# Kernel optimization log

Hardware: AMD Instinct MI355X
Metric: run time of the kernel (lower is better)

Reference implementation:

```python
import jax, jax.numpy as jnp
import numpy as np

N_HEADS = 32
D_IN = 128 + 256 + 1024  # 1408
D_HID = 256
D_OUT = 3


def setup_inputs() -> dict:
    key = jax.random.key(0)
    k1, k2, k3, k4, k5 = jax.random.split(key, 5)
    B = 16384
    total_feat = jax.random.normal(k1, (B, D_IN), dtype=jnp.float32)
    # Stacked per-head parameters. Original zero-inits the second Linear;
    # we use small random values so the baseline exercises non-trivial math.
    s1 = 1.0 / np.sqrt(D_IN)
    s2 = 1.0 / np.sqrt(D_HID)
    W1 = jax.random.uniform(k2, (N_HEADS, D_IN, D_HID), jnp.float32, -s1, s1)
    b1 = jax.random.uniform(k3, (N_HEADS, D_HID), jnp.float32, -s1, s1)
    W2 = jax.random.uniform(k4, (N_HEADS, D_HID, D_OUT), jnp.float32, -s2, s2)
    b2 = jax.random.uniform(k5, (N_HEADS, D_OUT), jnp.float32, -s2, s2)
    return {"total_feat": total_feat, "W1": W1, "b1": b1, "W2": W2, "b2": b2}


def reference(total_feat, W1, b1, W2, b2):
    # 32 heads of Linear(1408->256) -> ReLU -> Linear(256->3), batched.
    h = jax.nn.relu(jnp.einsum('bf,hfo->bho', total_feat, W1) + b1)  # [B,32,256]
    out = jnp.einsum('bho,hop->bhp', h, W2) + b2                     # [B,32,3]
    B = total_feat.shape[0]
    # concat(dim=-1) over heads == reshape since each head emits 3 contiguous values
    return out.reshape(B, N_HEADS * D_OUT)                           # [B,96]
```

## Files before the change

### kernel.cpp

```cpp
#include <hip/hip_runtime.h>
#include <hip/hip_bf16.h>
#include <stdint.h>

#define D_IN    1408
#define D_HID   256
#define N_HEADS 32
#define BATCH   16384

#define BM 128
#define BN 256
#define BK 32
#define KTILES (D_IN / BK)
#define NSEG 8

typedef unsigned short u16;
typedef short short8 __attribute__((ext_vector_type(8)));
typedef float f32x4 __attribute__((ext_vector_type(4)));

__device__ __forceinline__ u16 f2b(float f) {
  __hip_bfloat16 h = __float2bfloat16(f);
  return *(u16*)&h;
}

__device__ __forceinline__ void gload_lds16(const void* g, void* l) {
  __builtin_amdgcn_global_load_lds(
      (const __attribute__((address_space(1))) uint32_t*)((const uint32_t*)g),
      (__attribute__((address_space(3))) uint32_t*)((uint32_t*)l),
      16, 0, 0);
}

#define CONV_BLOCKS 22528
__global__ void prep(const float4* __restrict__ X, ushort4* __restrict__ Xb,
                     const float* __restrict__ W1, u16* __restrict__ W1T) {
  const int bid = blockIdx.x;
  const int tid = threadIdx.x;
  if (bid < CONV_BLOCKS) {
    int i = bid * 256 + tid;
    float4 v = X[i];
    ushort4 o;
    o.x = f2b(v.x); o.y = f2b(v.y); o.z = f2b(v.z); o.w = f2b(v.w);
    Xb[i] = o;
    return;
  }
  __shared__ u16 tile[64][68];
  const int b  = bid - CONV_BLOCKS;
  const int f0 = (b % 22) * 64;
  const int o0 = ((b / 22) & 3) * 64;
  const int h  = b / 88;
  const int tx = tid & 63;
  const int ty = tid >> 6;
  const size_t ib = (size_t)h * D_IN * D_HID;
  #pragma unroll
  for (int i = ty; i < 64; i += 4)
    tile[i][tx] = f2b(W1[ib + (size_t)(f0 + i) * D_HID + o0 + tx]);
  __syncthreads();
  const size_t ob = (size_t)h * D_HID * D_IN;
  #pragma unroll
  for (int pass = 0; pass < 4; ++pass) {
    int r = pass * 16 + ty * 4 + (tx >> 4);
    int c = (tx & 15) * 4;
    ushort4 v;
    v.x = tile[c + 0][r]; v.y = tile[c + 1][r];
    v.z = tile[c + 2][r]; v.w = tile[c + 3][r];
    *(ushort4*)&W1T[ob + (size_t)(o0 + r) * D_IN + f0 + c] = v;
  }
}

__global__ __launch_bounds__(512, 4) void mano_gemm(
    const u16* __restrict__ X,
    const u16* __restrict__ W1T,
    const float* __restrict__ b1,
    const float* __restrict__ W2,
    const float* __restrict__ b2,
    float* __restrict__ out)
{
  __shared__ __align__(16) u16 As[2][BM * BK];
  __shared__ __align__(16) u16 Bs[2][BN * BK];
  __shared__ __align__(16) float scr[1536];
  __shared__ float b1L[256];
  __shared__ float w2L[768];
  __shared__ float b2L[3];

  const int tid  = threadIdx.x;
  const int lane = tid & 63;
  const int wid  = tid >> 6;
  const int quad = lane >> 4;
  const int l15  = lane & 15;
  const int wm   = wid >> 2;
  const int wn   = wid & 3;

  const int bid  = blockIdx.x;
  const int head = (bid & 7) * 4 + ((bid >> 3) & 3);
  const int u    = bid >> 5;

  const u16* Bu = W1T + (size_t)head * D_HID * D_IN;

  if (tid < 256) b1L[tid] = b1[head * D_HID + tid];
  for (int i = tid; i < 768; i += 512) w2L[i] = W2[(size_t)head * D_HID * 3 + i];
  if (tid < 3)  b2L[tid] = b2[head * 3 + tid];

  int aoff;
  {
    int row = tid >> 2, c = tid & 3;
    aoff = row * D_IN + (c ^ ((row >> 1) & 3)) * 8;
  }
  int boff[2];
  #pragma unroll
  for (int cc = 0; cc < 2; ++cc) {
    int ci = cc * 512 + tid;
    int row = ci >> 2, c = ci & 3;
    boff[cc] = row * D_IN + (c ^ ((row >> 1) & 3)) * 8;
  }

  const int p16 = (quad ^ ((l15 >> 1) & 3)) * 16;
  const int abase = (wm * 64 + l15) * 64 + p16;
  const int bbase = (wn * 64 + l15) * 64 + p16;

#define STG(BI, AP, BP) do {                                                   \
    gload_lds16((AP) + aoff, &As[BI][wid * 512]);                              \
    _Pragma("unroll")                                                          \
    for (int cc = 0; cc < 2; ++cc)                                             \
      gload_lds16((BP) + boff[cc], &Bs[BI][(cc * 512 + wid * 64) * 8]);        \
  } while (0)

  f32x4 acc[4][4];
  #pragma unroll
  for (int i = 0; i < 4; ++i)
    #pragma unroll
    for (int j = 0; j < 4; ++j)
      acc[i][j] = f32x4{0.f, 0.f, 0.f, 0.f};

  short8 a[4], b[4];

#define TILE(BI, AP, BP, SK) do {                                              \
    if (!(SK)) STG((BI) ^ 1, AP, BP);                                          \
    _Pragma("unroll") for (int mf = 0; mf < 4; ++mf)                           \
      a[mf] = *(const short8*)((const char*)&As[BI][0] + abase + mf * 1024);   \
    _Pragma("unroll") for (int nf = 0; nf < 4; ++nf)                           \
      b[nf] = *(const short8*)((const char*)&Bs[BI][0] + bbase + nf * 1024);   \
    __builtin_amdgcn_s_setprio(1);                                             \
    _Pragma("unroll") for (int mf = 0; mf < 4; ++mf)                           \
      _Pragma("unroll") for (int nf = 0; nf < 4; ++nf)                         \
        acc[mf][nf] = __builtin_amdgcn_mfma_f32_16x16x32_bf16(                 \
            a[mf], b[nf], acc[mf][nf], 0, 0, 0);                               \
    __builtin_amdgcn_s_setprio(0);                                             \
    asm volatile("s_waitcnt vmcnt(0)" ::: "memory");                           \
    __builtin_amdgcn_s_barrier();                                              \
  } while (0)

  {
    const u16* A0 = X + (size_t)(u * BM) * D_IN;
    STG(0, A0, Bu);
    asm volatile("s_waitcnt lgkmcnt(0)" ::: "memory");
    asm volatile("s_waitcnt vmcnt(0)" ::: "memory");
    __builtin_amdgcn_s_barrier();
  }

  #pragma unroll 1
  for (int g = 0; g < NSEG; ++g) {
    const u16* AuC = X + (size_t)((g * 16 + u) * BM) * D_IN;
    const u16* AuN = AuC + (size_t)(16 * BM) * D_IN;
    const bool lastseg = (g == NSEG - 1);

    #pragma unroll 1
    for (int j = 0; j < KTILES / 2; ++j) {
      const int kt1 = 2 * j + 1;
      const int kt2 = 2 * j + 2;
      const bool wrap = (kt2 >= KTILES);
      const int k2m  = wrap ? 0 : kt2;
      const u16* Ap1 = AuC + kt1 * BK;
      const u16* Bp1 = Bu + kt1 * BK;
      const u16* Ap2 = (wrap ? AuN : AuC) + k2m * BK;
      const u16* Bp2 = Bu + k2m * BK;
      const bool sk2 = lastseg && wrap;

      TILE(0, Ap1, Bp1, false);
      TILE(1, Ap2, Bp2, sk2);
    }

    {
      float b1v[4], w2v[4][3];
      #pragma unroll
      for (int nf = 0; nf < 4; ++nf) {
        int col = wn * 64 + nf * 16 + l15;
        b1v[nf] = b1L[col];
        #pragma unroll
        for (int p = 0; p < 3; ++p) w2v[nf][p] = w2L[col * 3 + p];
      }
      const int m0 = (g * 16 + u) * BM;

      #pragma unroll
      for (int mf = 0; mf < 4; ++mf) {
        float ps[4][3];
        #pragma unroll
        for (int r = 0; r < 4; ++r)
          #pragma unroll
          for (int p = 0; p < 3; ++p) ps[r][p] = 0.f;

        #pragma unroll
        for (int nf = 0; nf < 4; ++nf)
          #pragma unroll
          for (int r = 0; r < 4; ++r) {
            float h = acc[mf][nf][r] + b1v[nf];
            h = h > 0.f ? h : 0.f;
            #pragma unroll
            for (int p = 0; p < 3; ++p)
              ps[r][p] = fmaf(h, w2v[nf][p], ps[r][p]);
          }

        #pragma unroll
        for (int mask = 1; mask < 16; mask <<= 1)
          #pragma unroll
          for (int r = 0; r < 4; ++r)
            #pragma unroll
            for (int p = 0; p < 3; ++p)
              ps[r][p] += __shfl_xor(ps[r][p], mask, 64);

        if (l15 == 0) {
          int row = wm * 64 + mf * 16 + quad * 4;
          #pragma unroll
          for (int r = 0; r < 4; ++r)
            #pragma unroll
            for (int p = 0; p < 3; ++p)
              scr[((row + r) * 3 + p) * 4 + wn] = ps[r][p];
        }
      }
      asm volatile("s_waitcnt lgkmcnt(0)" ::: "memory");
      __builtin_amdgcn_s_barrier();

      for (int i = tid; i < BM * 3; i += 512) {
        int row = i / 3, p = i - row * 3;
        float v = scr[i * 4 + 0] + scr[i * 4 + 1] + scr[i * 4 + 2]
                + scr[i * 4 + 3] + b2L[p];
        out[(size_t)(m0 + row) * (N_HEADS * 3) + head * 3 + p] = v;
      }

      #pragma unroll
      for (int i = 0; i < 4; ++i)
        #pragma unroll
        for (int jj = 0; jj < 4; ++jj)
          acc[i][jj] = f32x4{0.f, 0.f, 0.f, 0.f};
    }
  }

#undef STG
#undef TILE
}

extern "C" void kernel_launch(void* const* d_in, const int* in_sizes, int n_in,
                              void* d_out, int out_size, void* d_ws, size_t ws_size,
                              hipStream_t stream) {
  const float* X  = (const float*)d_in[0];
  const float* W1 = (const float*)d_in[1];
  const float* b1 = (const float*)d_in[2];
  const float* W2 = (const float*)d_in[3];
  const float* b2 = (const float*)d_in[4];

  u16* Xb  = (u16*)d_ws;
  u16* W1T = (u16*)((char*)d_ws + (size_t)BATCH * D_IN * 2);

  prep<<<CONV_BLOCKS + (D_IN / 64) * (D_HID / 64) * N_HEADS, 256, 0, stream>>>(
      (const float4*)X, (ushort4*)Xb, W1, W1T);

  mano_gemm<<<dim3(512), 512, 0, stream>>>(
      Xb, W1T, b1, W2, b2, (float*)d_out);
}
```

Measured before the change: 574.3 us.

## Enlarge GEMM block tile to 256x256x64 with 4 waves of 128x128 each

```diff
diff --git a/kernel.cpp b/kernel.cpp
--- a/kernel.cpp
+++ b/kernel.cpp
@@ -7,9 +7,9 @@
 #define N_HEADS 32
 #define BATCH   16384
 
-#define BM 128
+#define BM 256
 #define BN 256
-#define BK 32
+#define BK 64
 #define KTILES (D_IN / BK)
 #define NSEG 8
 
@@ -66,7 +66,7 @@
   }
 }
 
-__global__ __launch_bounds__(512, 4) void mano_gemm(
+__global__ __launch_bounds__(256, 1) void mano_gemm(
     const u16* __restrict__ X,
     const u16* __restrict__ W1T,
     const float* __restrict__ b1,
@@ -86,71 +86,83 @@
   const int wid  = tid >> 6;
   const int quad = lane >> 4;
   const int l15  = lane & 15;
-  const int wm   = wid >> 2;
-  const int wn   = wid & 3;
+  const int wm   = wid >> 1;
+  const int wn   = wid & 1;
 
   const int bid  = blockIdx.x;
   const int head = (bid & 7) * 4 + ((bid >> 3) & 3);
-  const int u    = bid >> 5;
+  const int u2   = bid >> 5;
 
   const u16* Bu = W1T + (size_t)head * D_HID * D_IN;
 
-  if (tid < 256) b1L[tid] = b1[head * D_HID + tid];
-  for (int i = tid; i < 768; i += 512) w2L[i] = W2[(size_t)head * D_HID * 3 + i];
-  if (tid < 3)  b2L[tid] = b2[head * 3 + tid];
-
-  int aoff;
-  {
-    int row = tid >> 2, c = tid & 3;
-    aoff = row * D_IN + (c ^ ((row >> 1) & 3)) * 8;
-  }
-  int boff[2];
-  #pragma unroll
-  for (int cc = 0; cc < 2; ++cc) {
-    int ci = cc * 512 + tid;
-    int row = ci >> 2, c = ci & 3;
-    boff[cc] = row * D_IN + (c ^ ((row >> 1) & 3)) * 8;
-  }
-
-  const int p16 = (quad ^ ((l15 >> 1) & 3)) * 16;
-  const int abase = (wm * 64 + l15) * 64 + p16;
-  const int bbase = (wn * 64 + l15) * 64 + p16;
-
-#define STG(BI, AP, BP) do {                                                   \
-    gload_lds16((AP) + aoff, &As[BI][wid * 512]);                              \
-    _Pragma("unroll")                                                          \
-    for (int cc = 0; cc < 2; ++cc)                                             \
-      gload_lds16((BP) + boff[cc], &Bs[BI][(cc * 512 + wid * 64) * 8]);        \
-  } while (0)
-
-  f32x4 acc[4][4];
-  #pragma unroll
-  for (int i = 0; i < 4; ++i)
+  b1L[tid] = b1[head * D_HID + tid];
+  #pragma unroll
+  for (int i = tid; i < 768; i += 256) w2L[i] = W2[(size_t)head * D_HID * 3 + i];
+  if (tid < 3) b2L[tid] = b2[head * 3 + tid];
+
+  int soff[8];
+  #pragma unroll
+  for (int c = 0; c < 8; ++c) {
+    int ci  = c * 256 + tid;
+    int row = ci >> 3;
+    int k8  = (ci & 7) ^ (row & 7);
+    soff[c] = row * D_IN + k8 * 8;
+  }
+
+#define STG_A(BI, P) do { _Pragma("unroll")                                    \
+    for (int c = 0; c < 8; ++c)                                                \
+      gload_lds16((P) + soff[c], &As[BI][(c * 256 + wid * 64) * 8]); } while (0)
+#define STG_B(BI, P) do { _Pragma("unroll")                                    \
+    for (int c = 0; c < 8; ++c)                                                \
+      gload_lds16((P) + soff[c], &Bs[BI][(c * 256 + wid * 64) * 8]); } while (0)
+
+  const int rx  = l15 & 7;
+  const int co0 = (quad ^ rx) * 16;
+  const int co1 = ((4 + quad) ^ rx) * 16;
+  const int aro = (wm * 128 + l15) * 128;
+  const int bro = (wn * 128 + l15) * 128;
+
+#define LDA(BI, mf, CO) \
+  (*(const short8*)((const char*)&As[BI][0] + aro + (mf) * 2048 + (CO)))
+#define LDB(BI, nf, CO) \
+  (*(const short8*)((const char*)&Bs[BI][0] + bro + (nf) * 2048 + (CO)))
+
+  f32x4 acc[8][8];
+  #pragma unroll
+  for (int i = 0; i < 8; ++i)
     #pragma unroll
-    for (int j = 0; j < 4; ++j)
+    for (int j = 0; j < 8; ++j)
       acc[i][j] = f32x4{0.f, 0.f, 0.f, 0.f};
 
-  short8 a[4], b[4];
-
-#define TILE(BI, AP, BP, SK) do {                                              \
-    if (!(SK)) STG((BI) ^ 1, AP, BP);                                          \
-    _Pragma("unroll") for (int mf = 0; mf < 4; ++mf)                           \
-      a[mf] = *(const short8*)((const char*)&As[BI][0] + abase + mf * 1024);   \
-    _Pragma("unroll") for (int nf = 0; nf < 4; ++nf)                           \
-      b[nf] = *(const short8*)((const char*)&Bs[BI][0] + bbase + nf * 1024);   \
+  short8 fa0[8], fb0[8], fa1[8], fb1[8];
+
+#define TILE(BI, APn, BPn, SK) do {                                            \
+    _Pragma("unroll") for (int m = 0; m < 8; ++m) fa0[m] = LDA(BI, m, co0);    \
+    _Pragma("unroll") for (int n = 0; n < 8; ++n) fb0[n] = LDB(BI, n, co0);    \
+    _Pragma("unroll") for (int m = 0; m < 8; ++m) fa1[m] = LDA(BI, m, co1);    \
+    _Pragma("unroll") for (int n = 0; n < 8; ++n) fb1[n] = LDB(BI, n, co1);    \
+    if (!(SK)) STG_A((BI) ^ 1, APn);                                           \
     __builtin_amdgcn_s_setprio(1);                                             \
-    _Pragma("unroll") for (int mf = 0; mf < 4; ++mf)                           \
-      _Pragma("unroll") for (int nf = 0; nf < 4; ++nf)                         \
-        acc[mf][nf] = __builtin_amdgcn_mfma_f32_16x16x32_bf16(                 \
-            a[mf], b[nf], acc[mf][nf], 0, 0, 0);                               \
+    _Pragma("unroll") for (int m = 0; m < 8; ++m)                              \
+      _Pragma("unroll") for (int n = 0; n < 8; ++n)                            \
+        acc[m][n] = __builtin_amdgcn_mfma_f32_16x16x32_bf16(                   \
+            fa0[m], fb0[n], acc[m][n], 0, 0, 0);                               \
+    __builtin_amdgcn_s_setprio(0);                                             \
+    if (!(SK)) STG_B((BI) ^ 1, BPn);                                           \
+    __builtin_amdgcn_s_setprio(1);                                             \
+    _Pragma("unroll") for (int m = 0; m < 8; ++m)                              \
+      _Pragma("unroll") for (int n = 0; n < 8; ++n)                            \
+        acc[m][n] = __builtin_amdgcn_mfma_f32_16x16x32_bf16(                   \
+            fa1[m], fb1[n], acc[m][n], 0, 0, 0);                               \
     __builtin_amdgcn_s_setprio(0);                                             \
     asm volatile("s_waitcnt vmcnt(0)" ::: "memory");                           \
     __builtin_amdgcn_s_barrier();                                              \
   } while (0)
 
   {
-    const u16* A0 = X + (size_t)(u * BM) * D_IN;
-    STG(0, A0, Bu);
+    const u16* A0 = X + (size_t)(u2 * BM) * D_IN;
+    STG_A(0, A0);
+    STG_B(0, Bu);
     asm volatile("s_waitcnt lgkmcnt(0)" ::: "memory");
     asm volatile("s_waitcnt vmcnt(0)" ::: "memory");
     __builtin_amdgcn_s_barrier();
@@ -158,39 +170,32 @@
 
   #pragma unroll 1
   for (int g = 0; g < NSEG; ++g) {
-    const u16* AuC = X + (size_t)((g * 16 + u) * BM) * D_IN;
-    const u16* AuN = AuC + (size_t)(16 * BM) * D_IN;
+    const u16* AuC = X + (size_t)((g * 8 + u2) * BM) * D_IN;
+    const u16* AuN = AuC + (size_t)(8 * BM) * D_IN;
     const bool lastseg = (g == NSEG - 1);
 
     #pragma unroll 1
     for (int j = 0; j < KTILES / 2; ++j) {
-      const int kt1 = 2 * j + 1;
-      const int kt2 = 2 * j + 2;
-      const bool wrap = (kt2 >= KTILES);
-      const int k2m  = wrap ? 0 : kt2;
-      const u16* Ap1 = AuC + kt1 * BK;
-      const u16* Bp1 = Bu + kt1 * BK;
-      const u16* Ap2 = (wrap ? AuN : AuC) + k2m * BK;
-      const u16* Bp2 = Bu + k2m * BK;
-      const bool sk2 = lastseg && wrap;
-
-      TILE(0, Ap1, Bp1, false);
-      TILE(1, Ap2, Bp2, sk2);
+      TILE(0, AuC + (2 * j + 1) * BK, Bu + (2 * j + 1) * BK, false);
+      const bool wrap = (j == KTILES / 2 - 1);
+      const u16* Ap2 = wrap ? AuN : AuC + (2 * j + 2) * BK;
+      const u16* Bp2 = Bu + (wrap ? 0 : (2 * j + 2)) * BK;
+      TILE(1, Ap2, Bp2, lastseg && wrap);
     }
 
     {
-      float b1v[4], w2v[4][3];
-      #pragma unroll
-      for (int nf = 0; nf < 4; ++nf) {
-        int col = wn * 64 + nf * 16 + l15;
-        b1v[nf] = b1L[col];
-        #pragma unroll
-        for (int p = 0; p < 3; ++p) w2v[nf][p] = w2L[col * 3 + p];
+      float b1v[8], w2v[8][3];
+      #pragma unroll
+      for (int n = 0; n < 8; ++n) {
+        int col = wn * 128 + n * 16 + l15;
+        b1v[n] = b1L[col];
+        #pragma unroll
+        for (int p = 0; p < 3; ++p) w2v[n][p] = w2L[col * 3 + p];
       }
-      const int m0 = (g * 16 + u) * BM;
-
-      #pragma unroll
-      for (int mf = 0; mf < 4; ++mf) {
+      const int m0 = (g * 8 + u2) * BM;
+
+      #pragma unroll
+      for (int m = 0; m < 8; ++m) {
         float ps[4][3];
         #pragma unroll
         for (int r = 0; r < 4; ++r)
@@ -198,14 +203,14 @@
           for (int p = 0; p < 3; ++p) ps[r][p] = 0.f;
 
         #pragma unroll
-        for (int nf = 0; nf < 4; ++nf)
+        for (int n = 0; n < 8; ++n)
           #pragma unroll
           for (int r = 0; r < 4; ++r) {
-            float h = acc[mf][nf][r] + b1v[nf];
+            float h = acc[m][n][r] + b1v[n];
             h = h > 0.f ? h : 0.f;
             #pragma unroll
             for (int p = 0; p < 3; ++p)
-              ps[r][p] = fmaf(h, w2v[nf][p], ps[r][p]);
+              ps[r][p] = fmaf(h, w2v[n][p], ps[r][p]);
           }
 
         #pragma unroll
@@ -217,33 +222,36 @@
               ps[r][p] += __shfl_xor(ps[r][p], mask, 64);
 
         if (l15 == 0) {
-          int row = wm * 64 + mf * 16 + quad * 4;
+          int row = wm * 128 + m * 16 + quad * 4;
           #pragma unroll
           for (int r = 0; r < 4; ++r)
             #pragma unroll
             for (int p = 0; p < 3; ++p)
-              scr[((row + r) * 3 + p) * 4 + wn] = ps[r][p];
+              scr[((row + r) * 3 + p) * 2 + wn] = ps[r][p];
         }
       }
       asm volatile("s_waitcnt lgkmcnt(0)" ::: "memory");
       __builtin_amdgcn_s_barrier();
 
-      for (int i = tid; i < BM * 3; i += 512) {
+      #pragma unroll
+      for (int i = tid; i < BM * 3; i += 256) {
         int row = i / 3, p = i - row * 3;
-        float v = scr[i * 4 + 0] + scr[i * 4 + 1] + scr[i * 4 + 2]
-                + scr[i * 4 + 3] + b2L[p];
-        out[(size_t)(m0 + row) * (N_HEADS * 3) + head * 3 + p] = v;
+        out[(size_t)(m0 + row) * (N_HEADS * 3) + head * 3 + p] =
+            scr[i * 2] + scr[i * 2 + 1] + b2L[p];
       }
 
       #pragma unroll
-      for (int i = 0; i < 4; ++i)
-        #pragma unroll
-        for (int jj = 0; jj < 4; ++jj)
+      for (int i = 0; i < 8; ++i)
+        #pragma unroll
+        for (int jj = 0; jj < 8; ++jj)
           acc[i][jj] = f32x4{0.f, 0.f, 0.f, 0.f};
     }
   }
 
-#undef STG
+#undef STG_A
+#undef STG_B
+#undef LDA
+#undef LDB
 #undef TILE
 }
 
@@ -262,6 +270,6 @@
   prep<<<CONV_BLOCKS + (D_IN / 64) * (D_HID / 64) * N_HEADS, 256, 0, stream>>>(
       (const float4*)X, (ushort4*)Xb, W1, W1T);
 
-  mano_gemm<<<dim3(512), 512, 0, stream>>>(
+  mano_gemm<<<dim3(256), 256, 0, stream>>>(
       Xb, W1T, b1, W2, b2, (float*)d_out);
 }
```

After: 1.022 ms. 1.78x slower.

## Triple-buffer LDS tiles with prefetch distance two and partial vmcnt waits

Applied to the files above, without the earlier changes.

```diff
diff --git a/kernel.cpp b/kernel.cpp
--- a/kernel.cpp
+++ b/kernel.cpp
@@ -12,6 +12,7 @@
 #define BK 32
 #define KTILES (D_IN / BK)
 #define NSEG 8
+#define BUFU16 (BM * BK + BN * BK)
 
 typedef unsigned short u16;
 typedef short short8 __attribute__((ext_vector_type(8)));
@@ -74,9 +75,7 @@
     const float* __restrict__ b2,
     float* __restrict__ out)
 {
-  __shared__ __align__(16) u16 As[2][BM * BK];
-  __shared__ __align__(16) u16 Bs[2][BN * BK];
-  __shared__ __align__(16) float scr[1536];
+  __shared__ __align__(16) u16 tiles[3][BUFU16];
   __shared__ float b1L[256];
   __shared__ float w2L[768];
   __shared__ float b2L[3];
@@ -94,6 +93,7 @@
   const int u    = bid >> 5;
 
   const u16* Bu = W1T + (size_t)head * D_HID * D_IN;
+  u16* lds = &tiles[0][0];
 
   if (tid < 256) b1L[tid] = b1[head * D_HID + tid];
   for (int i = tid; i < 768; i += 512) w2L[i] = W2[(size_t)head * D_HID * 3 + i];
@@ -116,11 +116,12 @@
   const int abase = (wm * 64 + l15) * 64 + p16;
   const int bbase = (wn * 64 + l15) * 64 + p16;
 
-#define STG(BI, AP, BP) do {                                                   \
-    gload_lds16((AP) + aoff, &As[BI][wid * 512]);                              \
+#define STG(BUFP, AP, BP) do {                                                 \
+    gload_lds16((AP) + aoff, (BUFP) + wid * 512);                              \
     _Pragma("unroll")                                                          \
     for (int cc = 0; cc < 2; ++cc)                                             \
-      gload_lds16((BP) + boff[cc], &Bs[BI][(cc * 512 + wid * 64) * 8]);        \
+      gload_lds16((BP) + boff[cc],                                             \
+                  (BUFP) + 4096 + cc * 4096 + wid * 512);                      \
   } while (0)
 
   f32x4 acc[4][4];
@@ -132,29 +133,16 @@
 
   short8 a[4], b[4];
 
-#define TILE(BI, AP, BP, SK) do {                                              \
-    if (!(SK)) STG((BI) ^ 1, AP, BP);                                          \
-    _Pragma("unroll") for (int mf = 0; mf < 4; ++mf)                           \
-      a[mf] = *(const short8*)((const char*)&As[BI][0] + abase + mf * 1024);   \
-    _Pragma("unroll") for (int nf = 0; nf < 4; ++nf)                           \
-      b[nf] = *(const short8*)((const char*)&Bs[BI][0] + bbase + nf * 1024);   \
-    __builtin_amdgcn_s_setprio(1);                                             \
-    _Pragma("unroll") for (int mf = 0; mf < 4; ++mf)                           \
-      _Pragma("unroll") for (int nf = 0; nf < 4; ++nf)                         \
-        acc[mf][nf] = __builtin_amdgcn_mfma_f32_16x16x32_bf16(                 \
-            a[mf], b[nf], acc[mf][nf], 0, 0, 0);                               \
-    __builtin_amdgcn_s_setprio(0);                                             \
-    asm volatile("s_waitcnt vmcnt(0)" ::: "memory");                           \
-    __builtin_amdgcn_s_barrier();                                              \
-  } while (0)
-
   {
     const u16* A0 = X + (size_t)(u * BM) * D_IN;
-    STG(0, A0, Bu);
+    STG(lds, A0, Bu);
+    STG(lds + BUFU16, A0 + BK, Bu + BK);
     asm volatile("s_waitcnt lgkmcnt(0)" ::: "memory");
-    asm volatile("s_waitcnt vmcnt(0)" ::: "memory");
+    asm volatile("s_waitcnt vmcnt(3)" ::: "memory");
     __builtin_amdgcn_s_barrier();
   }
+
+  int bq = 0;
 
   #pragma unroll 1
   for (int g = 0; g < NSEG; ++g) {
@@ -163,22 +151,46 @@
     const bool lastseg = (g == NSEG - 1);
 
     #pragma unroll 1
-    for (int j = 0; j < KTILES / 2; ++j) {
-      const int kt1 = 2 * j + 1;
-      const int kt2 = 2 * j + 2;
-      const bool wrap = (kt2 >= KTILES);
-      const int k2m  = wrap ? 0 : kt2;
-      const u16* Ap1 = AuC + kt1 * BK;
-      const u16* Bp1 = Bu + kt1 * BK;
-      const u16* Ap2 = (wrap ? AuN : AuC) + k2m * BK;
-      const u16* Bp2 = Bu + k2m * BK;
-      const bool sk2 = lastseg && wrap;
-
-      TILE(0, Ap1, Bp1, false);
-      TILE(1, Ap2, Bp2, sk2);
+    for (int kt = 0; kt < KTILES; ++kt) {
+      int k2 = kt + 2;
+      const u16* Ab2 = AuC;
+      bool skip = false;
+      if (k2 >= KTILES) { k2 -= KTILES; Ab2 = AuN; skip = lastseg; }
+      const bool drain = lastseg && (kt >= KTILES - 2);
+
+      int bq2 = bq + 2; if (bq2 >= 3) bq2 -= 3;
+      u16* bufC = lds + bq * BUFU16;
+      u16* bufN = lds + bq2 * BUFU16;
+
+      if (!skip) STG(bufN, Ab2 + k2 * BK, Bu + k2 * BK);
+
+      #pragma unroll
+      for (int mf = 0; mf < 4; ++mf)
+        a[mf] = *(const short8*)((const char*)bufC + abase + mf * 1024);
+      #pragma unroll
+      for (int nf = 0; nf < 4; ++nf)
+        b[nf] = *(const short8*)((const char*)bufC + 8192 + bbase + nf * 1024);
+
+      __builtin_amdgcn_s_setprio(1);
+      #pragma unroll
+      for (int mf = 0; mf < 4; ++mf)
+        #pragma unroll
+        for (int nf = 0; nf < 4; ++nf)
+          acc[mf][nf] = __builtin_amdgcn_mfma_f32_16x16x32_bf16(
+              a[mf], b[nf], acc[mf][nf], 0, 0, 0);
+      __builtin_amdgcn_s_setprio(0);
+
+      if (drain) { asm volatile("s_waitcnt vmcnt(0)" ::: "memory"); }
+      else       { asm volatile("s_waitcnt vmcnt(3)" ::: "memory"); }
+      __builtin_amdgcn_s_barrier();
+
+      bq = bq + 1; if (bq >= 3) bq -= 3;
     }
 
     {
+      int bqf = bq + 2; if (bqf >= 3) bqf -= 3;
+      float* scr = (float*)(lds + bqf * BUFU16);
+
       float b1v[4], w2v[4][3];
       #pragma unroll
       for (int nf = 0; nf < 4; ++nf) {
@@ -234,6 +246,7 @@
                 + scr[i * 4 + 3] + b2L[p];
         out[(size_t)(m0 + row) * (N_HEADS * 3) + head * 3 + p] = v;
       }
+      asm volatile("s_waitcnt lgkmcnt(0)" ::: "memory");
 
       #pragma unroll
       for (int i = 0; i < 4; ++i)
@@ -244,7 +257,6 @@
   }
 
 #undef STG
-#undef TILE
 }
 
 extern "C" void kernel_launch(void* const* d_in, const int* in_sizes, int n_in,
```

Measured after the change: 590.0 us. +2.7%, slower.

## Double GEMM M tile and K step, load weights directly into registers

Applied to the files above, without the earlier changes.

```diff
diff --git a/kernel.cpp b/kernel.cpp
--- a/kernel.cpp
+++ b/kernel.cpp
@@ -7,9 +7,9 @@
 #define N_HEADS 32
 #define BATCH   16384
 
-#define BM 128
+#define BM 256
 #define BN 256
-#define BK 32
+#define BK 64
 #define KTILES (D_IN / BK)
 #define NSEG 8
 
@@ -66,7 +66,7 @@
   }
 }
 
-__global__ __launch_bounds__(512, 4) void mano_gemm(
+__global__ __launch_bounds__(512, 2) void mano_gemm(
     const u16* __restrict__ X,
     const u16* __restrict__ W1T,
     const float* __restrict__ b1,
@@ -75,8 +75,7 @@
     float* __restrict__ out)
 {
   __shared__ __align__(16) u16 As[2][BM * BK];
-  __shared__ __align__(16) u16 Bs[2][BN * BK];
-  __shared__ __align__(16) float scr[1536];
+  __shared__ __align__(16) float scr[3072];
   __shared__ float b1L[256];
   __shared__ float w2L[768];
   __shared__ float b2L[3];
@@ -91,7 +90,7 @@
 
   const int bid  = blockIdx.x;
   const int head = (bid & 7) * 4 + ((bid >> 3) & 3);
-  const int u    = bid >> 5;
+  const int u2   = bid >> 5;
 
   const u16* Bu = W1T + (size_t)head * D_HID * D_IN;
 
@@ -99,58 +98,72 @@
   for (int i = tid; i < 768; i += 512) w2L[i] = W2[(size_t)head * D_HID * 3 + i];
   if (tid < 3)  b2L[tid] = b2[head * 3 + tid];
 
-  int aoff;
-  {
-    int row = tid >> 2, c = tid & 3;
-    aoff = row * D_IN + (c ^ ((row >> 1) & 3)) * 8;
-  }
-  int boff[2];
-  #pragma unroll
-  for (int cc = 0; cc < 2; ++cc) {
-    int ci = cc * 512 + tid;
-    int row = ci >> 2, c = ci & 3;
-    boff[cc] = row * D_IN + (c ^ ((row >> 1) & 3)) * 8;
-  }
-
-  const int p16 = (quad ^ ((l15 >> 1) & 3)) * 16;
-  const int abase = (wm * 64 + l15) * 64 + p16;
-  const int bbase = (wn * 64 + l15) * 64 + p16;
-
-#define STG(BI, AP, BP) do {                                                   \
-    gload_lds16((AP) + aoff, &As[BI][wid * 512]);                              \
-    _Pragma("unroll")                                                          \
-    for (int cc = 0; cc < 2; ++cc)                                             \
-      gload_lds16((BP) + boff[cc], &Bs[BI][(cc * 512 + wid * 64) * 8]);        \
-  } while (0)
-
-  f32x4 acc[4][4];
-  #pragma unroll
-  for (int i = 0; i < 4; ++i)
+  int soff[4];
+  #pragma unroll
+  for (int c = 0; c < 4; ++c) {
+    int ci  = c * 512 + tid;
+    int row = ci >> 3;
+    int k8  = (ci & 7) ^ (row & 7);
+    soff[c] = row * D_IN + k8 * 8;
+  }
+
+#define STG_A(BI, P) do { _Pragma("unroll")                                    \
+    for (int c = 0; c < 4; ++c)                                                \
+      gload_lds16((P) + soff[c], &As[BI][(c * 512 + wid * 64) * 8]); } while (0)
+
+  const int wm16l = wm * 16 + l15;
+  const int rx  = l15 & 7;
+  const int co0 = (quad ^ rx) * 16;
+  const int co1 = ((4 + quad) ^ rx) * 16;
+
+#define LDAF(BI, mf, CO)                                                       \
+  (*(const short8*)((const char*)&As[BI][0] + ((mf) * 32 + wm16l) * 128 + (CO)))
+
+  int bgo[4];
+  #pragma unroll
+  for (int nf = 0; nf < 4; ++nf)
+    bgo[nf] = (nf * 64 + wn * 16 + l15) * D_IN + quad * 8;
+
+  f32x4 acc[8][4];
+  #pragma unroll
+  for (int i = 0; i < 8; ++i)
     #pragma unroll
     for (int j = 0; j < 4; ++j)
       acc[i][j] = f32x4{0.f, 0.f, 0.f, 0.f};
 
-  short8 a[4], b[4];
-
-#define TILE(BI, AP, BP, SK) do {                                              \
-    if (!(SK)) STG((BI) ^ 1, AP, BP);                                          \
-    _Pragma("unroll") for (int mf = 0; mf < 4; ++mf)                           \
-      a[mf] = *(const short8*)((const char*)&As[BI][0] + abase + mf * 1024);   \
+  short8 a[8];
+  short8 bA[4][2], bB[4][2];
+
+#define TILE(BI, APn, SKA, BCUR, BNXT, KTB) do {                               \
     _Pragma("unroll") for (int nf = 0; nf < 4; ++nf)                           \
-      b[nf] = *(const short8*)((const char*)&Bs[BI][0] + bbase + nf * 1024);   \
+      _Pragma("unroll") for (int ks = 0; ks < 2; ++ks)                         \
+        BNXT[nf][ks] = *(const short8*)(Bu + bgo[nf] + (KTB) * BK + ks * 32);  \
+    if (!(SKA)) STG_A((BI) ^ 1, APn);                                          \
+    _Pragma("unroll") for (int mf = 0; mf < 8; ++mf) a[mf] = LDAF(BI, mf, co0);\
     __builtin_amdgcn_s_setprio(1);                                             \
-    _Pragma("unroll") for (int mf = 0; mf < 4; ++mf)                           \
+    _Pragma("unroll") for (int mf = 0; mf < 8; ++mf)                           \
       _Pragma("unroll") for (int nf = 0; nf < 4; ++nf)                         \
         acc[mf][nf] = __builtin_amdgcn_mfma_f32_16x16x32_bf16(                 \
-            a[mf], b[nf], acc[mf][nf], 0, 0, 0);                               \
+            a[mf], BCUR[nf][0], acc[mf][nf], 0, 0, 0);                         \
+    __builtin_amdgcn_s_setprio(0);                                             \
+    _Pragma("unroll") for (int mf = 0; mf < 8; ++mf) a[mf] = LDAF(BI, mf, co1);\
+    __builtin_amdgcn_s_setprio(1);                                             \
+    _Pragma("unroll") for (int mf = 0; mf < 8; ++mf)                           \
+      _Pragma("unroll") for (int nf = 0; nf < 4; ++nf)                         \
+        acc[mf][nf] = __builtin_amdgcn_mfma_f32_16x16x32_bf16(                 \
+            a[mf], BCUR[nf][1], acc[mf][nf], 0, 0, 0);                         \
     __builtin_amdgcn_s_setprio(0);                                             \
     asm volatile("s_waitcnt vmcnt(0)" ::: "memory");                           \
     __builtin_amdgcn_s_barrier();                                              \
   } while (0)
 
   {
-    const u16* A0 = X + (size_t)(u * BM) * D_IN;
-    STG(0, A0, Bu);
+    #pragma unroll
+    for (int nf = 0; nf < 4; ++nf)
+      #pragma unroll
+      for (int ks = 0; ks < 2; ++ks)
+        bA[nf][ks] = *(const short8*)(Bu + bgo[nf] + ks * 32);
+    STG_A(0, X + (size_t)(u2 * BM) * D_IN);
     asm volatile("s_waitcnt lgkmcnt(0)" ::: "memory");
     asm volatile("s_waitcnt vmcnt(0)" ::: "memory");
     __builtin_amdgcn_s_barrier();
@@ -158,39 +171,33 @@
 
   #pragma unroll 1
   for (int g = 0; g < NSEG; ++g) {
-    const u16* AuC = X + (size_t)((g * 16 + u) * BM) * D_IN;
-    const u16* AuN = AuC + (size_t)(16 * BM) * D_IN;
+    const u16* AuC = X + (size_t)((g * 8 + u2) * BM) * D_IN;
+    const u16* AuN = AuC + (size_t)(8 * BM) * D_IN;
     const bool lastseg = (g == NSEG - 1);
 
     #pragma unroll 1
     for (int j = 0; j < KTILES / 2; ++j) {
-      const int kt1 = 2 * j + 1;
-      const int kt2 = 2 * j + 2;
-      const bool wrap = (kt2 >= KTILES);
-      const int k2m  = wrap ? 0 : kt2;
-      const u16* Ap1 = AuC + kt1 * BK;
-      const u16* Bp1 = Bu + kt1 * BK;
-      const u16* Ap2 = (wrap ? AuN : AuC) + k2m * BK;
-      const u16* Bp2 = Bu + k2m * BK;
-      const bool sk2 = lastseg && wrap;
-
-      TILE(0, Ap1, Bp1, false);
-      TILE(1, Ap2, Bp2, sk2);
+      const int kt0 = 2 * j;
+      TILE(0, AuC + (kt0 + 1) * BK, false, bA, bB, kt0 + 1);
+      const bool wrap = (j == KTILES / 2 - 1);
+      const u16* Ap2 = wrap ? AuN : AuC + (kt0 + 2) * BK;
+      const int  kB2 = wrap ? 0 : kt0 + 2;
+      TILE(1, Ap2, lastseg && wrap, bB, bA, kB2);
     }
 
     {
       float b1v[4], w2v[4][3];
       #pragma unroll
       for (int nf = 0; nf < 4; ++nf) {
-        int col = wn * 64 + nf * 16 + l15;
+        int col = nf * 64 + wn * 16 + l15;
         b1v[nf] = b1L[col];
         #pragma unroll
         for (int p = 0; p < 3; ++p) w2v[nf][p] = w2L[col * 3 + p];
       }
-      const int m0 = (g * 16 + u) * BM;
-
-      #pragma unroll
-      for (int mf = 0; mf < 4; ++mf) {
+      const int m0 = (g * 8 + u2) * BM;
+
+      #pragma unroll
+      for (int mf = 0; mf < 8; ++mf) {
         float ps[4][3];
         #pragma unroll
         for (int r = 0; r < 4; ++r)
@@ -217,7 +224,7 @@
               ps[r][p] += __shfl_xor(ps[r][p], mask, 64);
 
         if (l15 == 0) {
-          int row = wm * 64 + mf * 16 + quad * 4;
+          int row = mf * 32 + wm * 16 + quad * 4;
           #pragma unroll
           for (int r = 0; r < 4; ++r)
             #pragma unroll
@@ -236,14 +243,15 @@
       }
 
       #pragma unroll
-      for (int i = 0; i < 4; ++i)
+      for (int i = 0; i < 8; ++i)
         #pragma unroll
         for (int jj = 0; jj < 4; ++jj)
           acc[i][jj] = f32x4{0.f, 0.f, 0.f, 0.f};
     }
   }
 
-#undef STG
+#undef STG_A
+#undef LDAF
 #undef TILE
 }
 
@@ -262,6 +270,6 @@
   prep<<<CONV_BLOCKS + (D_IN / 64) * (D_HID / 64) * N_HEADS, 256, 0, stream>>>(
       (const float4*)X, (ushort4*)Xb, W1, W1T);
 
-  mano_gemm<<<dim3(512), 512, 0, stream>>>(
+  mano_gemm<<<dim3(256), 512, 0, stream>>>(
       Xb, W1T, b1, W2, b2, (float*)d_out);
 }
```

New measurement: 1.216 ms. 112% more time.
